# Kernel tuning notes

Measured on AMD Instinct MI355X. Metric: run time of the kernel, lower is better.

The kernel has to match this reference:

```python
import jax, jax.numpy as jnp
import numpy as np

B, H, W, C = 64, 28, 28, 384
G = 7
N = G * G                  # tokens per window = 49
NH, HD = 12, 32            # heads, head_dim
SCALE = HD ** -0.5
EPS = 1e-5


def _make_bias_coords():
    # biases: all relative (dh, dw) offsets, shape [(2G-1)^2, 2]
    r = np.arange(1 - G, G)
    biases = np.stack(np.meshgrid(r, r, indexing='ij')).reshape(2, -1).T.astype(np.float32)
    # relative_position_index: [N, N] lookup into the bias table
    coords = np.stack(np.meshgrid(np.arange(G), np.arange(G), indexing='ij')).reshape(2, -1)
    rel = coords[:, :, None] - coords[:, None, :]          # [2, N, N]
    rel = rel.transpose(1, 2, 0)                            # [N, N, 2]
    rel[:, :, 0] += G - 1
    rel[:, :, 1] += G - 1
    rel[:, :, 0] *= 2 * G - 1
    idx = rel.sum(-1)                                       # [N, N]
    return jnp.asarray(biases), jnp.asarray(idx, dtype=jnp.int32)

BIASES, REL_IDX = _make_bias_coords()


def _ln(x, g, b):
    m = jnp.mean(x, -1, keepdims=True)
    v = jnp.var(x, -1, keepdims=True)
    return (x - m) * jax.lax.rsqrt(v + EPS) * g + b


def _pos_bias(ppw, ppb, l1g, l1b, p1w, p1b, l2g, l2b, p2w, p2b, l3g, l3b, p3w, p3b):
    # DynamicPosBias with residual=False: pos3(pos2(pos1(pos_proj(biases))))
    pos = BIASES @ ppw + ppb                                # [169, 24]
    pos = jax.nn.relu(_ln(pos, l1g, l1b)) @ p1w + p1b
    pos = jax.nn.relu(_ln(pos, l2g, l2b)) @ p2w + p2b
    pos = jax.nn.relu(_ln(pos, l3g, l3b)) @ p3w + p3b       # [169, NH]
    # gather -> [N, N, NH] -> [NH, N, N]
    return pos[REL_IDX.reshape(-1)].reshape(N, N, NH).transpose(2, 0, 1)


def _forward(x, norm1_g, norm1_b, qkv_w, qkv_b, proj_w, proj_b,
             norm2_g, norm2_b, fc1_w, fc1_b, fc2_w, fc2_b,
             pp_w, pp_b, l1_g, l1_b, p1_w, p1_b, l2_g, l2_b, p2_w, p2_b,
             l3_g, l3_b, p3_w, p3_b):
    shortcut = x
    h = _ln(x, norm1_g, norm1_b).reshape(B, H, W, C)
    # SDA (lsda_flag=0) window partition: [B, H/G, G, W/G, G, C] -> windows
    h = h.reshape(B, H // G, G, W // G, G, C).transpose(0, 1, 3, 2, 4, 5)
    h = h.reshape(-1, N, C)                                 # [B*nW, N, C]
    Bw = h.shape[0]

    qkv = (h @ qkv_w + qkv_b).reshape(Bw, N, 3, NH, HD).transpose(2, 0, 3, 1, 4)
    q, k, v = qkv[0] * SCALE, qkv[1], qkv[2]                # [Bw, NH, N, HD]

    bias = _pos_bias(pp_w, pp_b, l1_g, l1_b, p1_w, p1_b,
                     l2_g, l2_b, p2_w, p2_b, l3_g, l3_b, p3_w, p3_b)
    attn = jnp.einsum('bhnd,bhmd->bhnm', q, k) + bias[None]  # [Bw, NH, N, N]
    attn = jax.nn.softmax(attn, axis=-1)

    o = jnp.einsum('bhnm,bhmd->bhnd', attn, v)
    o = o.transpose(0, 2, 1, 3).reshape(Bw, N, C)
    o = o @ proj_w + proj_b

    # reverse window partition
    o = o.reshape(B, H // G, W // G, G, G, C).transpose(0, 1, 3, 2, 4, 5)
    o = o.reshape(B, H * W, C)

    x = shortcut + o
    y = _ln(x, norm2_g, norm2_b)
    y = jax.nn.gelu(y @ fc1_w + fc1_b, approximate=False) @ fc2_w + fc2_b
    return x + y


def setup_inputs() -> dict:
    key = jax.random.key(0)
    ks = iter(jax.random.split(key, 32))
    s = 0.02
    PD = 24  # pos_dim = (dim // 4) // 4
    MH = 4 * C

    def rn(k, shape):
        return jax.random.normal(k, shape, dtype=jnp.float32) * s

    return {
        'x': jax.random.normal(next(ks), (B, H * W, C), dtype=jnp.float32),
        'norm1_g': jnp.ones((C,), jnp.float32), 'norm1_b': jnp.zeros((C,), jnp.float32),
        'qkv_w': rn(next(ks), (C, 3 * C)), 'qkv_b': jnp.zeros((3 * C,), jnp.float32),
        'proj_w': rn(next(ks), (C, C)), 'proj_b': jnp.zeros((C,), jnp.float32),
        'norm2_g': jnp.ones((C,), jnp.float32), 'norm2_b': jnp.zeros((C,), jnp.float32),
        'fc1_w': rn(next(ks), (C, MH)), 'fc1_b': jnp.zeros((MH,), jnp.float32),
        'fc2_w': rn(next(ks), (MH, C)), 'fc2_b': jnp.zeros((C,), jnp.float32),
        'pp_w': rn(next(ks), (2, PD)), 'pp_b': jnp.zeros((PD,), jnp.float32),
        'l1_g': jnp.ones((PD,), jnp.float32), 'l1_b': jnp.zeros((PD,), jnp.float32),
        'p1_w': rn(next(ks), (PD, PD)), 'p1_b': jnp.zeros((PD,), jnp.float32),
        'l2_g': jnp.ones((PD,), jnp.float32), 'l2_b': jnp.zeros((PD,), jnp.float32),
        'p2_w': rn(next(ks), (PD, PD)), 'p2_b': jnp.zeros((PD,), jnp.float32),
        'l3_g': jnp.ones((PD,), jnp.float32), 'l3_b': jnp.zeros((PD,), jnp.float32),
        'p3_w': rn(next(ks), (PD, NH)), 'p3_b': jnp.zeros((NH,), jnp.float32),
    }


def reference(x, norm1_g, norm1_b, qkv_w, qkv_b, proj_w, proj_b,
              norm2_g, norm2_b, fc1_w, fc1_b, fc2_w, fc2_b,
              pp_w, pp_b, l1_g, l1_b, p1_w, p1_b, l2_g, l2_b, p2_w, p2_b,
              l3_g, l3_b, p3_w, p3_b):
    return _forward(x, norm1_g, norm1_b, qkv_w, qkv_b, proj_w, proj_b,
                    norm2_g, norm2_b, fc1_w, fc1_b, fc2_w, fc2_b,
                    pp_w, pp_b, l1_g, l1_b, p1_w, p1_b, l2_g, l2_b, p2_w, p2_b,
                    l3_g, l3_b, p3_w, p3_b)
```

## Files before the change

kernel.cpp:

```cpp
#include <hip/hip_runtime.h>

typedef unsigned short u16;
typedef short s16x8 __attribute__((ext_vector_type(8)));
typedef short s16x4 __attribute__((ext_vector_type(4)));
typedef float f32x4 __attribute__((ext_vector_type(4)));
typedef float f32x2 __attribute__((ext_vector_type(2)));

#define B_ 64
#define Hh 28
#define Ww 28
#define Cc 384
#define Gg 7
#define Nn 49
#define NH 12
#define HD 32
#define TT 50176
#define NWIN 1024
#define QKV_ELEMS 19267584u
#define SCALE_Q 0.17677669529663687f

__device__ __forceinline__ float b2f(u16 u) {
  union { unsigned int i; float f; } v; v.i = ((unsigned int)u) << 16; return v.f;
}
__device__ __forceinline__ u16 f2b(float f) {
  union { float f; unsigned int i; } v; v.f = f;
  unsigned int r = v.i + 0x7fffu + ((v.i >> 16) & 1u);
  return (u16)(r >> 16);
}

__device__ __forceinline__ void gload_lds16(const u16* g, u16* l) {
  __builtin_amdgcn_global_load_lds(
      (const __attribute__((address_space(1))) unsigned int*)(const void*)g,
      (__attribute__((address_space(3))) unsigned int*)(void*)l, 16, 0, 0);
}

__global__ void transpose_f2b(const float* __restrict__ in, u16* __restrict__ out,
                              int K, int N) {
  int i = blockIdx.x * 256 + threadIdx.x;
  if (i < K * N) {
    int k = i / N, n = i % N;
    out[(size_t)n * K + k] = f2b(in[i]);
  }
}

__global__ __launch_bounds__(256)
void pos_mlp_kernel(const float* __restrict__ pp_w, const float* __restrict__ pp_b,
                    const float* __restrict__ l1g, const float* __restrict__ l1b,
                    const float* __restrict__ p1w, const float* __restrict__ p1b,
                    const float* __restrict__ l2g, const float* __restrict__ l2b,
                    const float* __restrict__ p2w, const float* __restrict__ p2b,
                    const float* __restrict__ l3g, const float* __restrict__ l3b,
                    const float* __restrict__ p3w, const float* __restrict__ p3b,
                    float* __restrict__ pos169) {
  __shared__ float w0[48], bb0[24], g1[24], e1[24], w1[576], bb1[24],
                   g2[24], e2[24], w2[576], bb2[24], g3[24], e3[24], w3[288], bb3[12];
  int tid = threadIdx.x;
  for (int i = tid; i < 48; i += 256) w0[i] = pp_w[i];
  for (int i = tid; i < 24; i += 256) {
    bb0[i] = pp_b[i]; g1[i] = l1g[i]; e1[i] = l1b[i]; bb1[i] = p1b[i];
    g2[i] = l2g[i]; e2[i] = l2b[i]; bb2[i] = p2b[i];
    g3[i] = l3g[i]; e3[i] = l3b[i];
  }
  for (int i = tid; i < 576; i += 256) { w1[i] = p1w[i]; w2[i] = p2w[i]; }
  for (int i = tid; i < 288; i += 256) w3[i] = p3w[i];
  for (int i = tid; i < 12; i += 256) bb3[i] = p3b[i];
  __syncthreads();
  if (tid < 169) {
    float bi = (float)(tid / 13) - 6.f, bj = (float)(tid % 13) - 6.f;
    float cur[24], t[24];
    #pragma unroll
    for (int c = 0; c < 24; c++) cur[c] = bi * w0[c] + bj * w0[24 + c] + bb0[c];

    auto lnrelu = [&](const float* gg, const float* ee) {
      float s = 0.f, sq = 0.f;
      #pragma unroll
      for (int c = 0; c < 24; c++) { s += cur[c]; sq += cur[c] * cur[c]; }
      float mean = s * (1.f / 24.f);
      float var = sq * (1.f / 24.f) - mean * mean;
      float rstd = rsqrtf(var + 1e-5f);
      #pragma unroll
      for (int c = 0; c < 24; c++)
        t[c] = fmaxf(0.f, (cur[c] - mean) * rstd * gg[c] + ee[c]);
    };

    lnrelu(g1, e1);
    #pragma unroll
    for (int o = 0; o < 24; o++) {
      float a = bb1[o];
      #pragma unroll
      for (int c = 0; c < 24; c++) a += t[c] * w1[c * 24 + o];
      cur[o] = a;
    }
    lnrelu(g2, e2);
    #pragma unroll
    for (int o = 0; o < 24; o++) {
      float a = bb2[o];
      #pragma unroll
      for (int c = 0; c < 24; c++) a += t[c] * w2[c * 24 + o];
      cur[o] = a;
    }
    lnrelu(g3, e3);
    #pragma unroll
    for (int h = 0; h < 12; h++) {
      float a = bb3[h];
      #pragma unroll
      for (int c = 0; c < 24; c++) a += t[c] * w3[c * 12 + h];
      pos169[tid * 12 + h] = a;
    }
  }
}

__global__ __launch_bounds__(256)
void ln_kernel(const float* __restrict__ x, const float* __restrict__ g,
               const float* __restrict__ be, u16* __restrict__ out) {
  int wid = threadIdx.x >> 6, lane = threadIdx.x & 63;
  size_t row = (size_t)blockIdx.x * 4 + wid;
  const float* xr = x + row * Cc;
  float v[6];
  float s = 0.f, sq = 0.f;
  #pragma unroll
  for (int p = 0; p < 3; p++) {
    f32x2 u = *(const f32x2*)&xr[p * 128 + lane * 2];
    v[2 * p] = u.x; v[2 * p + 1] = u.y;
    s += u.x + u.y; sq += u.x * u.x + u.y * u.y;
  }
  #pragma unroll
  for (int off = 32; off > 0; off >>= 1) { s += __shfl_xor(s, off); sq += __shfl_xor(sq, off); }
  float mean = s * (1.f / 384.f);
  float var = sq * (1.f / 384.f) - mean * mean;
  float rstd = rsqrtf(var + 1e-5f);
  u16* orow = out + row * Cc;
  #pragma unroll
  for (int p = 0; p < 3; p++) {
    int c = p * 128 + lane * 2;
    f32x2 ug = *(const f32x2*)&g[c];
    f32x2 ub = *(const f32x2*)&be[c];
    float o0 = (v[2 * p] - mean) * rstd * ug.x + ub.x;
    float o1 = (v[2 * p + 1] - mean) * rstd * ug.y + ub.y;
    unsigned int uo = (unsigned int)f2b(o0) | ((unsigned int)f2b(o1) << 16);
    *(unsigned int*)&orow[c] = uo;
  }
}

template <int EPI>
__global__ __launch_bounds__(256, 4)
void gemm_k(const u16* __restrict__ A, const u16* __restrict__ Bt,
            const float* __restrict__ bias, const void* resv, void* outv,
            int K, int gridX, int rowoff) {
  __shared__ u16 As[128 * 32];
  __shared__ u16 Bs[128 * 32];
  const int tid = threadIdx.x;
  const int wid = tid >> 6, lane = tid & 63;
  const int wr = (wid >> 1) * 64, wc = (wid & 1) * 64;
  const int lm = lane & 15, lq = lane >> 4;

  {
  }
  const int total = gridDim.x;
  const int xcd = blockIdx.x & 7, pos = blockIdx.x >> 3;
  const int cbase = total >> 3, crem = total & 7;
  const int tile = (xcd < crem) ? (xcd * (cbase + 1) + pos)
                                : (crem * (cbase + 1) + (xcd - crem) * cbase + pos);
  const int mTile = tile / gridX;
  const int nTile = tile - mTile * gridX;
  const int mBase = mTile * 128, nBase = nTile * 128;

  const int srow = tid >> 2;
  const int sg = (tid & 3) ^ ((tid >> 3) & 3);
  const size_t aRow0 = (size_t)(mBase + srow) * K + sg * 8;
  const size_t aRow1 = (size_t)(mBase + 64 + srow) * K + sg * 8;
  const size_t bRow0 = (size_t)(nBase + srow) * K + sg * 8;
  const size_t bRow1 = (size_t)(nBase + 64 + srow) * K + sg * 8;
  u16* aDst0 = As + tid * 8;
  u16* aDst1 = As + 2048 + tid * 8;
  u16* bDst0 = Bs + tid * 8;
  u16* bDst1 = Bs + 2048 + tid * 8;

  int aslot[4], bslot[4];
  #pragma unroll
  for (int i = 0; i < 4; i++) {
    int ar = wr + i * 16 + lm;
    aslot[i] = ar * 32 + (lq ^ ((ar >> 1) & 3)) * 8;
    int br = wc + i * 16 + lm;
    bslot[i] = br * 32 + (lq ^ ((br >> 1) & 3)) * 8;
  }

  f32x4 acc[4][4] = {};
  for (int k0 = 0; k0 < K; k0 += 32) {
    gload_lds16(A + aRow0 + k0, aDst0);
    gload_lds16(A + aRow1 + k0, aDst1);
    gload_lds16(Bt + bRow0 + k0, bDst0);
    gload_lds16(Bt + bRow1 + k0, bDst1);
    __syncthreads();
    s16x8 af[4], bfr[4];
    #pragma unroll
    for (int i = 0; i < 4; i++) af[i] = *(const s16x8*)&As[aslot[i]];
    #pragma unroll
    for (int j = 0; j < 4; j++) bfr[j] = *(const s16x8*)&Bs[bslot[j]];
    #pragma unroll
    for (int i = 0; i < 4; i++)
      #pragma unroll
      for (int j = 0; j < 4; j++)
        acc[i][j] = __builtin_amdgcn_mfma_f32_16x16x32_bf16(af[i], bfr[j], acc[i][j], 0, 0, 0);
    __syncthreads();
  }

  int colA[4]; float bvv[4];
  #pragma unroll
  for (int j = 0; j < 4; j++) {
    colA[j] = nBase + wc + j * 16 + lm;
    bvv[j] = bias[colA[j]];
  }

  if constexpr (EPI == 0) {
    u16* out = (u16*)outv;
    size_t offj[4]; float scl[4];
    #pragma unroll
    for (int j = 0; j < 4; j++) {
      int col = colA[j];
      int qi = col / 384, c2 = col % 384;
      int head = c2 >> 5, d = c2 & 31;
      offj[j] = (size_t)qi * QKV_ELEMS + (size_t)head * 1568 + d;
      scl[j] = (qi == 0) ? SCALE_Q : 1.0f;
    }
    #pragma unroll
    for (int i = 0; i < 4; i++) {
      #pragma unroll
      for (int rg = 0; rg < 4; rg++) {
        int t = mBase + wr + i * 16 + lq * 4 + rg;
        int b_ = t / 784, rr = t % 784;
        int hh = rr / 28, ww = rr % 28;
        int widx = b_ * 16 + (hh / 7) * 4 + (ww / 7);
        int n = (hh % 7) * 7 + (ww % 7);
        size_t offr = (size_t)widx * 18816 + n * 32;
        #pragma unroll
        for (int j = 0; j < 4; j++)
          out[offj[j] + offr] = f2b((acc[i][j][rg] + bvv[j]) * scl[j]);
      }
    }
  } else if constexpr (EPI == 1) {
    float* out = (float*)outv;
    const float* res = (const float*)resv;
    #pragma unroll
    for (int i = 0; i < 4; i++) {
      #pragma unroll
      for (int rg = 0; rg < 4; rg++) {
        size_t rb = (size_t)(rowoff + mBase + wr + i * 16 + lq * 4 + rg) * 384;
        #pragma unroll
        for (int j = 0; j < 4; j++) {
          size_t o = rb + colA[j];
          out[o] = acc[i][j][rg] + bvv[j] + res[o];
        }
      }
    }
  } else {
    u16* out = (u16*)outv;
    #pragma unroll
    for (int i = 0; i < 4; i++) {
      #pragma unroll
      for (int rg = 0; rg < 4; rg++) {
        size_t rb = (size_t)(mBase + wr + i * 16 + lq * 4 + rg) * 1536;
        #pragma unroll
        for (int j = 0; j < 4; j++) {
          float v = acc[i][j][rg] + bvv[j];
          float gl = 0.5f * v * (1.0f + erff(v * 0.70710678118654752f));
          out[rb + colA[j]] = f2b(gl);
        }
      }
    }
  }
}

__global__ __launch_bounds__(256, 3)
void attn_mfma(const u16* __restrict__ qkv, const float* __restrict__ pos169,
               u16* __restrict__ attn_out) {
  __shared__ u16 P_l[4][64 * 68];
  __shared__ float bias_l[4][170];
  const int wid = threadIdx.x >> 6, lane = threadIdx.x & 63;
  const int lm = lane & 15, lq = lane >> 4;
  const int pair = blockIdx.x * 4 + wid;
  const int widx = pair / 12, head = pair % 12;
  const u16* qp = qkv + (size_t)widx * 18816 + head * 1568;
  const u16* kp = qp + QKV_ELEMS;
  const u16* vp = kp + QKV_ELEMS;

  for (int i = lane; i < 169; i += 64) bias_l[wid][i] = pos169[i * 12 + head];

  s16x8 aq[4], bk[4];
  #pragma unroll
  for (int i = 0; i < 4; i++) aq[i] = *(const s16x8*)&qp[(i * 16 + lm) * 32 + lq * 8];
  #pragma unroll
  for (int j = 0; j < 4; j++) bk[j] = *(const s16x8*)&kp[(j * 16 + lm) * 32 + lq * 8];

  f32x4 acc[4][4] = {};
  #pragma unroll
  for (int i = 0; i < 4; i++)
    #pragma unroll
    for (int j = 0; j < 4; j++)
      acc[i][j] = __builtin_amdgcn_mfma_f32_16x16x32_bf16(aq[i], bk[j], acc[i][j], 0, 0, 0);

  int mj[4], mhj[4], mwj[4];
  #pragma unroll
  for (int j = 0; j < 4; j++) {
    mj[j] = j * 16 + lm; mhj[j] = mj[j] / 7; mwj[j] = mj[j] - mhj[j] * 7;
  }

  #pragma unroll
  for (int i = 0; i < 4; i++) {
    #pragma unroll
    for (int rg = 0; rg < 4; rg++) {
      int n = i * 16 + lq * 4 + rg;
      int nh = n / 7, nw = n - nh * 7;
      float s[4];
      #pragma unroll
      for (int j = 0; j < 4; j++) {
        int idx = (nh - mhj[j] + 6) * 13 + (nw - mwj[j] + 6);
        idx = min(max(idx, 0), 168);
        s[j] = acc[i][j][rg] + bias_l[wid][idx];
        if (mj[j] >= 49) s[j] = -3.0e30f;
      }
      float mx = fmaxf(fmaxf(s[0], s[1]), fmaxf(s[2], s[3]));
      #pragma unroll
      for (int off = 1; off < 16; off <<= 1) mx = fmaxf(mx, __shfl_xor(mx, off));
      float e[4];
      float sm = 0.f;
      #pragma unroll
      for (int j = 0; j < 4; j++) { e[j] = __expf(s[j] - mx); sm += e[j]; }
      #pragma unroll
      for (int off = 1; off < 16; off <<= 1) sm += __shfl_xor(sm, off);
      float r = 1.0f / sm;
      #pragma unroll
      for (int j = 0; j < 4; j++)
        P_l[wid][n * 68 + mj[j]] = f2b(e[j] * r);
    }
  }

  s16x8 ap[4][2];
  #pragma unroll
  for (int i = 0; i < 4; i++)
    #pragma unroll
    for (int ks = 0; ks < 2; ks++) {
      const u16* p = &P_l[wid][(i * 16 + lm) * 68 + ks * 32 + lq * 8];
      s16x4 lo = *(const s16x4*)p;
      s16x4 hi = *(const s16x4*)(p + 4);
      ap[i][ks] = __builtin_shufflevector(lo, hi, 0, 1, 2, 3, 4, 5, 6, 7);
    }
  s16x8 bv[2][2];
  #pragma unroll
  for (int jt = 0; jt < 2; jt++)
    #pragma unroll
    for (int ks = 0; ks < 2; ks++) {
      s16x8 v;
      #pragma unroll
      for (int jj = 0; jj < 8; jj++)
        v[jj] = (short)vp[(ks * 32 + lq * 8 + jj) * 32 + jt * 16 + lm];
      bv[jt][ks] = v;
    }

  f32x4 o[4][2] = {};
  #pragma unroll
  for (int i = 0; i < 4; i++)
    #pragma unroll
    for (int jt = 0; jt < 2; jt++)
      #pragma unroll
      for (int ks = 0; ks < 2; ks++)
        o[i][jt] = __builtin_amdgcn_mfma_f32_16x16x32_bf16(ap[i][ks], bv[jt][ks], o[i][jt], 0, 0, 0);

  const int b_ = widx >> 4, wq = widx & 15;
  const int hbase = (wq >> 2) * 7, wbase = (wq & 3) * 7;
  #pragma unroll
  for (int i = 0; i < 4; i++) {
    #pragma unroll
    for (int rg = 0; rg < 4; rg++) {
      int n = i * 16 + lq * 4 + rg;
      if (n < 49) {
        int nh = n / 7, nw = n - nh * 7;
        int t = b_ * 784 + (hbase + nh) * 28 + (wbase + nw);
        size_t ob = (size_t)t * 384 + head * 32 + lm;
        attn_out[ob] = f2b(o[i][0][rg]);
        attn_out[ob + 16] = f2b(o[i][1][rg]);
      }
    }
  }
}

extern "C" void kernel_launch(void* const* d_in, const int* in_sizes, int n_in,
                              void* d_out, int out_size, void* d_ws, size_t ws_size,
                              hipStream_t stream) {
  const float* x      = (const float*)d_in[0];
  const float* n1g    = (const float*)d_in[1];
  const float* n1b    = (const float*)d_in[2];
  const float* qkv_w  = (const float*)d_in[3];
  const float* qkv_b  = (const float*)d_in[4];
  const float* proj_w = (const float*)d_in[5];
  const float* proj_b = (const float*)d_in[6];
  const float* n2g    = (const float*)d_in[7];
  const float* n2b    = (const float*)d_in[8];
  const float* fc1_w  = (const float*)d_in[9];
  const float* fc1_b  = (const float*)d_in[10];
  const float* fc2_w  = (const float*)d_in[11];
  const float* fc2_b  = (const float*)d_in[12];

  const size_t SZ_A = 115605504;
  const size_t SZ_B = 38535168;
  char* wsb = (char*)d_ws;
  u16* regA     = (u16*)wsb;
  u16* regB     = (u16*)(wsb + SZ_A);
  float* pos169 = (float*)(wsb + SZ_A + SZ_B);
  u16* qkvT     = (u16*)(wsb + SZ_A + SZ_B + 8192);
  u16* projT    = qkvT + 442368;
  u16* fc1T     = projT + 147456;
  u16* fc2T     = fc1T + 589824;

  float* out = (float*)d_out;

  transpose_f2b<<<1728, 256, 0, stream>>>(qkv_w, qkvT, 384, 1152);
  transpose_f2b<<<576, 256, 0, stream>>>(proj_w, projT, 384, 384);
  transpose_f2b<<<2304, 256, 0, stream>>>(fc1_w, fc1T, 384, 1536);
  transpose_f2b<<<2304, 256, 0, stream>>>(fc2_w, fc2T, 1536, 384);

  pos_mlp_kernel<<<1, 256, 0, stream>>>(
      (const float*)d_in[13], (const float*)d_in[14], (const float*)d_in[15], (const float*)d_in[16],
      (const float*)d_in[17], (const float*)d_in[18], (const float*)d_in[19], (const float*)d_in[20],
      (const float*)d_in[21], (const float*)d_in[22], (const float*)d_in[23], (const float*)d_in[24],
      (const float*)d_in[25], (const float*)d_in[26], pos169);

  ln_kernel<<<TT / 4, 256, 0, stream>>>(x, n1g, n1b, regB);

  gemm_k<0><<<392 * 9, 256, 0, stream>>>(regB, qkvT, qkv_b, nullptr, regA,
                                         384, 9, 0);

  attn_mfma<<<NWIN * NH / 4, 256, 0, stream>>>(regA, pos169, regB);

  gemm_k<1><<<392 * 3, 256, 0, stream>>>(regB, projT, proj_b, x, out,
                                         384, 3, 0);

  ln_kernel<<<TT / 4, 256, 0, stream>>>(out, n2g, n2b, regB);

  for (int ch = 0; ch < 2; ch++) {
    const u16* h2c = regB + (size_t)ch * 25088 * 384;
    gemm_k<2><<<196 * 12, 256, 0, stream>>>(h2c, fc1T, fc1_b, nullptr, regA,
                                            384, 12, 0);
    gemm_k<1><<<196 * 3, 256, 0, stream>>>(regA, fc2T, fc2_b, out, out,
                                           1536, 3, ch * 25088);
  }
}
```

Before: 664.2 us.

## Double-buffer GEMM LDS tiles and merge weight transpose launches

The GEMM kernel now keeps two LDS buffers for A and B and issues the global-to-LDS loads for the next K-slice before computing on the current one, so memory latency can overlap with MFMA work. The four weight transpose/convert launches are combined into one kernel that picks its matrix by block index, cutting launch overhead. Doubling the GEMM's shared memory may reduce occupancy. The per-iteration barrier structure stays largely the same.

New measurement: 656.6 us. No clear change (-1.2%).

```diff
diff --git a/kernel.cpp b/kernel.cpp
--- a/kernel.cpp
+++ b/kernel.cpp
@@ -34,9 +34,17 @@
       (__attribute__((address_space(3))) unsigned int*)(void*)l, 16, 0, 0);
 }
 
-__global__ void transpose_f2b(const float* __restrict__ in, u16* __restrict__ out,
-                              int K, int N) {
-  int i = blockIdx.x * 256 + threadIdx.x;
+__global__ void transpose_all(const float* __restrict__ w0, u16* __restrict__ o0,
+                              const float* __restrict__ w1, u16* __restrict__ o1,
+                              const float* __restrict__ w2, u16* __restrict__ o2,
+                              const float* __restrict__ w3, u16* __restrict__ o3) {
+  int b = blockIdx.x;
+  const float* in; u16* out; int K, N, base;
+  if (b < 1728)      { in = w0; out = o0; K = 384;  N = 1152; base = b; }
+  else if (b < 2304) { in = w1; out = o1; K = 384;  N = 384;  base = b - 1728; }
+  else if (b < 4608) { in = w2; out = o2; K = 384;  N = 1536; base = b - 2304; }
+  else               { in = w3; out = o3; K = 1536; N = 384;  base = b - 4608; }
+  int i = base * 256 + threadIdx.x;
   if (i < K * N) {
     int k = i / N, n = i % N;
     out[(size_t)n * K + k] = f2b(in[i]);
@@ -147,15 +155,13 @@
 void gemm_k(const u16* __restrict__ A, const u16* __restrict__ Bt,
             const float* __restrict__ bias, const void* resv, void* outv,
             int K, int gridX, int rowoff) {
-  __shared__ u16 As[128 * 32];
-  __shared__ u16 Bs[128 * 32];
+  __shared__ u16 As[2][4096];
+  __shared__ u16 Bs[2][4096];
   const int tid = threadIdx.x;
   const int wid = tid >> 6, lane = tid & 63;
   const int wr = (wid >> 1) * 64, wc = (wid & 1) * 64;
   const int lm = lane & 15, lq = lane >> 4;
 
-  {
-  }
   const int total = gridDim.x;
   const int xcd = blockIdx.x & 7, pos = blockIdx.x >> 3;
   const int cbase = total >> 3, crem = total & 7;
@@ -171,10 +177,6 @@
   const size_t aRow1 = (size_t)(mBase + 64 + srow) * K + sg * 8;
   const size_t bRow0 = (size_t)(nBase + srow) * K + sg * 8;
   const size_t bRow1 = (size_t)(nBase + 64 + srow) * K + sg * 8;
-  u16* aDst0 = As + tid * 8;
-  u16* aDst1 = As + 2048 + tid * 8;
-  u16* bDst0 = Bs + tid * 8;
-  u16* bDst1 = Bs + 2048 + tid * 8;
 
   int aslot[4], bslot[4];
   #pragma unroll
@@ -185,18 +187,25 @@
     bslot[i] = br * 32 + (lq ^ ((br >> 1) & 3)) * 8;
   }
 
+  auto stage = [&](int k0, int b) {
+    gload_lds16(A + aRow0 + k0, As[b] + tid * 8);
+    gload_lds16(A + aRow1 + k0, As[b] + 2048 + tid * 8);
+    gload_lds16(Bt + bRow0 + k0, Bs[b] + tid * 8);
+    gload_lds16(Bt + bRow1 + k0, Bs[b] + 2048 + tid * 8);
+  };
+
+  const int kIters = K >> 5;
   f32x4 acc[4][4] = {};
-  for (int k0 = 0; k0 < K; k0 += 32) {
-    gload_lds16(A + aRow0 + k0, aDst0);
-    gload_lds16(A + aRow1 + k0, aDst1);
-    gload_lds16(Bt + bRow0 + k0, bDst0);
-    gload_lds16(Bt + bRow1 + k0, bDst1);
-    __syncthreads();
+  stage(0, 0);
+  __syncthreads();
+  for (int k = 0; k < kIters; k++) {
+    const int cb = k & 1;
+    if (k + 1 < kIters) stage((k + 1) << 5, cb ^ 1);
     s16x8 af[4], bfr[4];
     #pragma unroll
-    for (int i = 0; i < 4; i++) af[i] = *(const s16x8*)&As[aslot[i]];
-    #pragma unroll
-    for (int j = 0; j < 4; j++) bfr[j] = *(const s16x8*)&Bs[bslot[j]];
+    for (int i = 0; i < 4; i++) af[i] = *(const s16x8*)&As[cb][aslot[i]];
+    #pragma unroll
+    for (int j = 0; j < 4; j++) bfr[j] = *(const s16x8*)&Bs[cb][bslot[j]];
     #pragma unroll
     for (int i = 0; i < 4; i++)
       #pragma unroll
@@ -414,10 +423,8 @@
 
   float* out = (float*)d_out;
 
-  transpose_f2b<<<1728, 256, 0, stream>>>(qkv_w, qkvT, 384, 1152);
-  transpose_f2b<<<576, 256, 0, stream>>>(proj_w, projT, 384, 384);
-  transpose_f2b<<<2304, 256, 0, stream>>>(fc1_w, fc1T, 384, 1536);
-  transpose_f2b<<<2304, 256, 0, stream>>>(fc2_w, fc2T, 1536, 384);
+  transpose_all<<<6912, 256, 0, stream>>>(qkv_w, qkvT, proj_w, projT,
+                                          fc1_w, fc1T, fc2_w, fc2T);
 
   pos_mlp_kernel<<<1, 256, 0, stream>>>(
       (const float*)d_in[13], (const float*)d_in[14], (const float*)d_in[15], (const float*)d_in[16],
```
